# Kernel tuning notes

Hardware: AMD Instinct MI355X
Metric: run time of the kernel (lower is better)

Reference implementation:

```python
import jax, jax.numpy as jnp
import numpy as np


def _leaky(x):
    return jnp.where(x > 0, x, 0.2 * x)


def _time_warp(x, strength, k_wp, k_sh):
    # Vectorized equivalent of the per-sample python loop in _apply_time_warp.
    B, L, Fd = x.shape
    warp_steps = (L * 0.1 * strength).astype(jnp.int32)
    wp = jax.random.randint(k_wp, (B, 1), warp_steps, L - warp_steps)
    sh = jax.random.randint(k_sh, (B, 1), -warp_steps, warp_steps + 1)
    t = jnp.arange(L)[None, :]
    # shift > 0: warped[t] = x[min(t+shift, L-1)] for t >= warp_point, else x[t]
    pos = jnp.where(t >= wp, jnp.minimum(t + sh, L - 1), t)
    # shift < 0: warped[t] = x[t - shift] for warp_point+shift <= t < L+shift, else x[t]
    neg = jnp.where((t >= wp + sh) & (t < L + sh), t - sh, t)
    idx = jnp.where(sh > 0, pos, jnp.where(sh < 0, neg, t))  # (B, L)
    warped = x[jnp.arange(B)[:, None], idx]  # gather along time -> (B, L, Fd)
    return warped


def _freq_aug(x, strength, k_f):
    fx = jnp.fft.fft(x, axis=1)
    ratio = jnp.minimum(strength * 0.1, 0.5)
    keep = jax.random.uniform(k_f, x.shape) > ratio
    res = jnp.fft.ifft(fx * keep.astype(fx.dtype), axis=1).real.astype(x.dtype)
    return jnp.where(strength < 0.01, x, res)


def _forward(x, batch_size, w1, b1, w2, b2, w3, b3, wm, bm, wn, bn, ws, bs,
             p_mask, p_noise, p_shift, p_scale):
    B, L, Fd = x.shape
    s_mask = jax.nn.sigmoid(p_mask)
    s_noise = jax.nn.sigmoid(p_noise)
    s_shift = jax.nn.sigmoid(p_shift)
    s_scale = jax.nn.sigmoid(p_scale)
    s_mix = 1.0 - s_shift

    key = jax.random.key(42)
    kz, kn, kwp, ksh, kf = jax.random.split(key, 5)

    z = jax.random.normal(kz, (B, w1.shape[0]), x.dtype)
    h = _leaky(z @ w1 + b1)
    h = _leaky(h @ w2 + b2)
    h = _leaky(h @ w3 + b3)  # (B, 2*hidden)

    mask = jax.nn.sigmoid(h @ wm + bm).reshape(B, L, Fd)
    mask = 1.0 - (1.0 - mask) * s_mask * 0.3

    noise_mag = jax.nn.softplus(h @ wn + bn).reshape(B, L, Fd)
    noise = jax.random.normal(kn, x.shape, x.dtype) * noise_mag * s_noise * 0.05

    warped = _time_warp(x, s_shift, kwp, ksh)

    scale = jax.nn.softplus(h @ ws + bs)[:, None, :]  # (B,1,Fd)
    scale = 1.0 + (scale - 0.5) * 0.2 * s_scale

    freq = _freq_aug(x, s_mix, kf)

    wa = jnp.clip(1.0 - s_mix - s_shift, 0.1, 0.8)
    wb = s_mix * 0.5
    wc = s_shift * 0.5
    tot = wa + wb + wc
    wa, wb, wc = wa / tot, wb / tot, wc / tot

    aug = x * mask * scale + noise
    aug = aug * wa + freq * wb + warped * wc
    return aug


def setup_inputs() -> dict:
    key = jax.random.key(0)
    ks = jax.random.split(key, 8)
    B, L, Fd = 256, 512, 64
    H, ND = 128, 64
    x = jax.random.normal(ks[0], (B, L, Fd), jnp.float32)

    def lin(k, i, o):
        return jax.random.normal(k, (i, o), jnp.float32) * 0.02

    inp = {
        "x": x,
        "batch_size": B,
        "w1": lin(ks[1], ND, H), "b1": jnp.zeros((H,), jnp.float32),
        "w2": lin(ks[2], H, 2 * H), "b2": jnp.zeros((2 * H,), jnp.float32),
        "w3": lin(ks[3], 2 * H, 2 * H), "b3": jnp.zeros((2 * H,), jnp.float32),
        "wm": lin(ks[4], 2 * H, L * Fd), "bm": jnp.zeros((L * Fd,), jnp.float32),
        "wn": lin(ks[5], 2 * H, L * Fd), "bn": jnp.zeros((L * Fd,), jnp.float32),
        "ws": lin(ks[6], 2 * H, Fd), "bs": jnp.zeros((Fd,), jnp.float32),
        "p_mask": jnp.float32(0.5), "p_noise": jnp.float32(0.5),
        "p_shift": jnp.float32(0.5), "p_scale": jnp.float32(0.5),
    }
    return inp


def reference(x, batch_size, w1, b1, w2, b2, w3, b3, wm, bm, wn, bn, ws, bs,
              p_mask, p_noise, p_shift, p_scale):
    return _forward(x, batch_size, w1, b1, w2, b2, w3, b3, wm, bm, wn, bn,
                    ws, bs, p_mask, p_noise, p_shift, p_scale)
```

## Files before the change

kernel.cpp:

```cpp
#include <hip/hip_runtime.h>
#include <cstdint>
#include <cstddef>


typedef unsigned int u32;
typedef unsigned short u16;

#define Bd 256
#define Ld 512
#define Fd 64
#define Nd 32768

struct U2 { u32 a, b; };

__device__ __forceinline__ u32 rotl32(u32 x, int r){ return (x << r) | (x >> (32 - r)); }

__device__ __forceinline__ U2 tf2x32(u32 k0, u32 k1, u32 x0, u32 x1){
  u32 ks2 = k0 ^ k1 ^ 0x1BD11BDAu;
  x0 += k0; x1 += k1;
#define TFR4(r0,r1,r2,r3) \
  x0 += x1; x1 = rotl32(x1, r0); x1 ^= x0; \
  x0 += x1; x1 = rotl32(x1, r1); x1 ^= x0; \
  x0 += x1; x1 = rotl32(x1, r2); x1 ^= x0; \
  x0 += x1; x1 = rotl32(x1, r3); x1 ^= x0;
  TFR4(13,15,26,6)  x0 += k1;  x1 += ks2 + 1u;
  TFR4(17,29,16,24) x0 += ks2; x1 += k0 + 2u;
  TFR4(13,15,26,6)  x0 += k0;  x1 += k1 + 3u;
  TFR4(17,29,16,24) x0 += k1;  x1 += ks2 + 4u;
  TFR4(13,15,26,6)  x0 += ks2; x1 += k0 + 5u;
#undef TFR4
  U2 r; r.a = x0; r.b = x1; return r;
}

__device__ __forceinline__ u32 rb32(u32 k0, u32 k1, u32 i){
  U2 r = tf2x32(k0, k1, 0u, i);
  return r.a ^ r.b;
}

__device__ __forceinline__ U2 split_key(u32 k0, u32 k1, u32 j){
  return tf2x32(k0, k1, 0u, j);
}

__device__ __forceinline__ float sigmoidf_(float x){ return 1.0f / (1.0f + expf(-x)); }
__device__ __forceinline__ float softplusf_(float x){ return fmaxf(x, 0.0f) + log1pf(expf(-fabsf(x))); }
__device__ __forceinline__ float leakyf_(float x){ return (x > 0.0f) ? x : 0.2f * x; }

__device__ __forceinline__ float erfinvf_(float x){
  float w = -log1pf(-x * x);
  float p;
  if (w < 5.0f){
    w -= 2.5f;
    p =               2.81022636e-08f;
    p = fmaf(p, w,    3.43273939e-07f);
    p = fmaf(p, w,   -3.5233877e-06f);
    p = fmaf(p, w,   -4.39150654e-06f);
    p = fmaf(p, w,    0.00021858087f);
    p = fmaf(p, w,   -0.00125372503f);
    p = fmaf(p, w,   -0.00417768164f);
    p = fmaf(p, w,    0.246640727f);
    p = fmaf(p, w,    1.50140941f);
  } else {
    w = sqrtf(w) - 3.0f;
    p =              -0.000200214257f;
    p = fmaf(p, w,    0.000100950558f);
    p = fmaf(p, w,    0.00134934322f);
    p = fmaf(p, w,   -0.00367342844f);
    p = fmaf(p, w,    0.00573950773f);
    p = fmaf(p, w,   -0.0076224613f);
    p = fmaf(p, w,    0.00943887047f);
    p = fmaf(p, w,    1.00167406f);
    p = fmaf(p, w,    2.83297682f);
  }
  return p * x;
}

__device__ __forceinline__ float uniform_from_bits(u32 bits){
  return __uint_as_float((bits >> 9) | 0x3f800000u) - 1.0f;
}

__device__ __forceinline__ float normal_from_bits(u32 bits){
  float u01 = uniform_from_bits(bits);
  const float lo = -0.99999994f;
  float v = fmaf(u01, 2.0f, lo);
  v = fmaxf(lo, v);
  return 1.41421356f * erfinvf_(v);
}

__device__ __forceinline__ int warp_idx_(int t, int wp, int sh){
  int tps = t + sh;
  int pos = (t >= wp) ? ((tps < Ld - 1) ? tps : (Ld - 1)) : t;
  int neg = ((t >= wp + sh) && (t < Ld + sh)) ? (t - sh) : t;
  return (sh > 0) ? pos : ((sh < 0) ? neg : t);
}

__device__ __forceinline__ u32 pack_bf16_2(float a, float b){
  u32 ua = __float_as_uint(a), ub = __float_as_uint(b);
  u32 ra = (ua + 0x7FFFu + ((ua >> 16) & 1u)) >> 16;
  u32 rb = (ub + 0x7FFFu + ((ub >> 16) & 1u)) >> 16;
  return (ra & 0xFFFFu) | (rb << 16);
}
__device__ __forceinline__ u16 f2bf(float a){
  u32 ua = __float_as_uint(a);
  return (u16)((ua + 0x7FFFu + ((ua >> 16) & 1u)) >> 16);
}
__device__ __forceinline__ float bf2f(u16 v){
  return __uint_as_float(((u32)v) << 16);
}

__device__ __forceinline__ int swz_(int v){
  return ((v >> 2) & 7) ^ ((v & 3) << 1);
}
__device__ __forceinline__ int rev9_(int k){
  return (int)(__brev((u32)k) >> 23);
}

__global__ __launch_bounds__(256) void k_mlp(
    const float* __restrict__ w1, const float* __restrict__ b1,
    const float* __restrict__ w2, const float* __restrict__ b2,
    const float* __restrict__ w3, const float* __restrict__ b3,
    const float* __restrict__ wsc, const float* __restrict__ bsc,
    const float* __restrict__ p_scale, const float* __restrict__ p_shift,
    u16* __restrict__ h3b, float* __restrict__ scl,
    int* __restrict__ wp, int* __restrict__ shv)
{
  __shared__ float zs[64];
  __shared__ float h1s[128];
  __shared__ float h2s[256];
  __shared__ float hs[256];
  int b = blockIdx.x, n = threadIdx.x;

  if (n < 64){
    U2 kz = split_key(0u, 42u, 0u);
    zs[n] = normal_from_bits(rb32(kz.a, kz.b, (u32)(b * 64 + n)));
  }
  __syncthreads();

  if (n < 128){
    float acc = b1[n];
    #pragma unroll 8
    for (int k = 0; k < 64; ++k) acc = fmaf(zs[k], w1[k * 128 + n], acc);
    h1s[n] = leakyf_(acc);
  }
  __syncthreads();

  {
    float acc = b2[n];
    #pragma unroll 8
    for (int k = 0; k < 128; ++k) acc = fmaf(h1s[k], w2[k * 256 + n], acc);
    h2s[n] = leakyf_(acc);
  }
  __syncthreads();

  {
    float acc = b3[n];
    #pragma unroll 8
    for (int k = 0; k < 256; ++k) acc = fmaf(h2s[k], w3[k * 256 + n], acc);
    u16 hv = f2bf(leakyf_(acc));
    h3b[b * 256 + n] = hv;
    hs[n] = bf2f(hv);
  }
  __syncthreads();

  if (n < 64){
    float a2 = bsc[n];
    for (int k = 0; k < 256; ++k) a2 = fmaf(hs[k], wsc[k * 64 + n], a2);
    float s_scale = sigmoidf_(p_scale[0]);
    scl[b * 64 + n] = 1.0f + (softplusf_(a2) - 0.5f) * 0.2f * s_scale;
  }

  if (b < 2 && n < 128){
    int bb = b * 128 + n;
    float s_shift = sigmoidf_(p_shift[0]);
    int wsteps = (int)(51.2f * s_shift);
    U2 kwp = split_key(0u, 42u, 2u);
    U2 ksh = split_key(0u, 42u, 3u);
    {
      U2 k1 = split_key(kwp.a, kwp.b, 0u);
      U2 k2 = split_key(kwp.a, kwp.b, 1u);
      u32 hi = rb32(k1.a, k1.b, (u32)bb);
      u32 lo = rb32(k2.a, k2.b, (u32)bb);
      u32 span = (u32)(Ld - 2 * wsteps);
      u32 mult = 65536u % span; mult = (mult * mult) % span;
      u32 off = ((hi % span) * mult + (lo % span)) % span;
      wp[bb] = wsteps + (int)off;
    }
    {
      U2 k1 = split_key(ksh.a, ksh.b, 0u);
      U2 k2 = split_key(ksh.a, ksh.b, 1u);
      u32 hi = rb32(k1.a, k1.b, (u32)bb);
      u32 lo = rb32(k2.a, k2.b, (u32)bb);
      u32 span = (u32)(2 * wsteps + 1);
      u32 mult = 65536u % span; mult = (mult * mult) % span;
      u32 off = ((hi % span) * mult + (lo % span)) % span;
      shv[bb] = -wsteps + (int)off;
    }
  }
}

typedef short short8 __attribute__((ext_vector_type(8)));
typedef float f32x4 __attribute__((ext_vector_type(4)));
union Frag { uint4 u; short8 s; };

__global__ __launch_bounds__(256, 2) void k_gemm(
    const u16* __restrict__ h3b,
    const float* __restrict__ wm, const float* __restrict__ bm,
    const float* __restrict__ wn, const float* __restrict__ bn,
    u32* __restrict__ mn)
{
  __shared__ __align__(16) u32 As [128 * 32];
  __shared__ __align__(16) u32 Bs0[128 * 32];
  __shared__ __align__(16) u32 Bs1[128 * 32];

  const int tid  = threadIdx.x;
  const int lane = tid & 63;
  const int w    = tid >> 6;
  const int q    = lane >> 4;
  const int lo   = lane & 15;
  const int nt0  = blockIdx.x << 7;
  const int b0   = blockIdx.y << 7;
  const int wr   = (w >> 1) << 6;
  const int wc   = (w & 1) << 6;

  const int p  = lane >> 3;
  const int c8 = lane & 7;
  const int nb = (w << 5) + (p << 2);

  f32x4 accm[4][4], accn[4][4];
  #pragma unroll
  for (int i = 0; i < 4; ++i)
    #pragma unroll
    for (int j = 0; j < 4; ++j){ accm[i][j] = (f32x4)0.0f; accn[i][j] = (f32x4)0.0f; }

  for (int kc = 0; kc < 256; kc += 64){
    if (kc) __syncthreads();
    #pragma unroll
    for (int j = 0; j < 4; ++j){
      int idx  = j * 256 + tid;
      int row  = idx >> 3;
      int slot = idx & 7;
      int g    = slot ^ swz_(row);
      uint4 v  = *(const uint4*)(h3b + (size_t)(b0 + row) * 256 + kc + g * 8);
      *(uint4*)&As[row * 32 + slot * 4] = v;
    }
    #pragma unroll
    for (int cp = 0; cp < 4; ++cp){
      int c = cp * 8 + c8;
      size_t gb = (size_t)(kc + 2 * c) * Nd + nt0 + nb;
      float4 m0 = *(const float4*)(wm + gb);
      float4 m1 = *(const float4*)(wm + gb + Nd);
      float4 v0 = *(const float4*)(wn + gb);
      float4 v1 = *(const float4*)(wn + gb + Nd);
      int g = c >> 2, cl = c & 3;
      #pragma unroll
      for (int s = 0; s < 4; ++s){
        int n = nb + s;
        int addr = n * 32 + (g ^ swz_(n)) * 4 + cl;
        float a0 = (s == 0) ? m0.x : (s == 1) ? m0.y : (s == 2) ? m0.z : m0.w;
        float a1 = (s == 0) ? m1.x : (s == 1) ? m1.y : (s == 2) ? m1.z : m1.w;
        float b0f = (s == 0) ? v0.x : (s == 1) ? v0.y : (s == 2) ? v0.z : v0.w;
        float b1f = (s == 0) ? v1.x : (s == 1) ? v1.y : (s == 2) ? v1.z : v1.w;
        Bs0[addr] = pack_bf16_2(a0, a1);
        Bs1[addr] = pack_bf16_2(b0f, b1f);
      }
    }
    __syncthreads();

    #pragma unroll
    for (int u = 0; u < 2; ++u){
      int G = u * 4 + q;
      Frag af[4], bfm[4], bfn[4];
      #pragma unroll
      for (int mt = 0; mt < 4; ++mt){
        int row = wr + mt * 16 + lo;
        af[mt].u = *(const uint4*)&As[row * 32 + (G ^ swz_(row)) * 4];
      }
      #pragma unroll
      for (int nt = 0; nt < 4; ++nt){
        int n = wc + nt * 16 + lo;
        int ad = n * 32 + (G ^ swz_(n)) * 4;
        bfm[nt].u = *(const uint4*)&Bs0[ad];
        bfn[nt].u = *(const uint4*)&Bs1[ad];
      }
      #pragma unroll
      for (int mt = 0; mt < 4; ++mt){
        #pragma unroll
        for (int nt = 0; nt < 4; ++nt){
          accm[mt][nt] = __builtin_amdgcn_mfma_f32_16x16x32_bf16(af[mt].s, bfm[nt].s, accm[mt][nt], 0, 0, 0);
          accn[mt][nt] = __builtin_amdgcn_mfma_f32_16x16x32_bf16(af[mt].s, bfn[nt].s, accn[mt][nt], 0, 0, 0);
        }
      }
    }
  }

  #pragma unroll
  for (int nt = 0; nt < 4; ++nt){
    int n = nt0 + wc + nt * 16 + lo;
    float bmv = bm[n];
    float bnv = bn[n];
    #pragma unroll
    for (int mt = 0; mt < 4; ++mt){
      #pragma unroll
      for (int r = 0; r < 4; ++r){
        int b = b0 + wr + mt * 16 + q * 4 + r;
        size_t o = (size_t)b * Nd + n;
        mn[o] = pack_bf16_2(accm[mt][nt][r] + bmv, accn[mt][nt][r] + bnv);
      }
    }
  }
}

__global__ __launch_bounds__(256) void k_noise(u32* __restrict__ mn,
                                               const float* __restrict__ p_noise){
  int gid = blockIdx.x * 256 + threadIdx.x;
  u32 base = (u32)gid * 8u;
  float s_noise = sigmoidf_(p_noise[0]);
  float sc = s_noise * 0.05f;
  U2 knk = split_key(0u, 42u, 1u);

  uint4 v0 = *(const uint4*)(mn + base);
  uint4 v1 = *(const uint4*)(mn + base + 4);
  u32 wds[8] = {v0.x, v0.y, v0.z, v0.w, v1.x, v1.y, v1.z, v1.w};
  #pragma unroll
  for (int h = 0; h < 8; ++h){
    u16 logit = (u16)(wds[h] >> 16);
    float nm = softplusf_(bf2f(logit));
    float nz = normal_from_bits(rb32(knk.a, knk.b, base + (u32)h));
    wds[h] = (wds[h] & 0xFFFFu) | ((u32)f2bf(nz * nm * sc) << 16);
  }
  *(uint4*)(mn + base)     = make_uint4(wds[0], wds[1], wds[2], wds[3]);
  *(uint4*)(mn + base + 4) = make_uint4(wds[4], wds[5], wds[6], wds[7]);
}

#define PITCH 529

__device__ __forceinline__ int lphys(int t){ return t + (t >> 5); }

__global__ __launch_bounds__(256, 4) void k_faug(
    const float* __restrict__ x,
    u32* mn,
    const float* __restrict__ scl,
    const int* __restrict__ wp, const int* __restrict__ shv,
    const float* __restrict__ p_mask, const float* __restrict__ p_noise,
    const float* __restrict__ p_shift)
{
  __shared__ float SR[8 * PITCH];
  __shared__ float SI[8 * PITCH];
  __shared__ float2 tw[256];

  const int tid = threadIdx.x;
  const int b   = blockIdx.x >> 2;
  const int f0  = (blockIdx.x & 3) << 4;

  float s_mask  = sigmoidf_(p_mask[0]);
  float s_shift = sigmoidf_(p_shift[0]);
  float s_mix   = 1.0f - s_shift;
  float ratio   = fminf(s_mix * 0.1f, 0.5f);
  float wa = 1.0f - s_mix - s_shift;
  wa = fminf(fmaxf(wa, 0.1f), 0.8f);
  float wb = s_mix * 0.5f;
  float wc = s_shift * 0.5f;
  float tot = wa + wb + wc;
  wa /= tot; wb /= tot; wc /= tot;
  bool pass = (s_mix < 0.01f);
  (void)p_noise;

  U2 kf  = split_key(0u, 42u, 4u);
  const int wpb = wp[b];
  const int shb = shv[b];

  {
    float ang = -6.283185307179586f * ((float)tid / 512.0f);
    tw[tid] = make_float2(cosf(ang), sinf(ang));
  }

  const float* xb = x + (size_t)b * Nd;
  #pragma unroll
  for (int s = 0; s < 8; ++s){
    int qq = (s << 8) + tid;
    int t  = qq >> 2;
    int f4 = qq & 3;
    float4 v = *(const float4*)(xb + t * 64 + f0 + (f4 << 2));
    int j = f4 << 1;
    int pt = lphys(t);
    SR[j * PITCH + pt]       = v.x;  SI[j * PITCH + pt]       = v.y;
    SR[(j + 1) * PITCH + pt] = v.z;  SI[(j + 1) * PITCH + pt] = v.w;
  }
  __syncthreads();

  for (int s = 9; s >= 1; --s){
    int half = 1 << (s - 1);
    #pragma unroll
    for (int it = 0; it < 8; ++it){
      int j  = it;
      int bi = tid;
      int pos = bi & (half - 1);
      int g = bi >> (s - 1);
      int i1 = (g << s) + pos;
      int i2 = i1 + half;
      int a1 = j * PITCH + lphys(i1);
      int a2 = j * PITCH + lphys(i2);
      float ur = SR[a1], ui = SI[a1];
      float vr = SR[a2], vi = SI[a2];
      SR[a1] = ur + vr; SI[a1] = ui + vi;
      float dr = ur - vr, di = ui - vi;
      float2 w = tw[pos << (9 - s)];
      SR[a2] = dr * w.x - di * w.y;
      SI[a2] = dr * w.y + di * w.x;
    }
    __syncthreads();
  }

  #pragma unroll
  for (int it = 0; it < 8; ++it){
    int j = it;
    int k = tid;
    int nItr = (k == 0) ? 2 : 1;
    for (int e = 0; e < nItr; ++e){
      int kk = (e == 0) ? k : 256;
      int nk = (512 - kk) & 511;
      int pk = rev9_(kk), pn = rev9_(nk);
      int ak = j * PITCH + lphys(pk);
      int an = j * PITCH + lphys(pn);
      float zkr = SR[ak], zki = SI[ak];
      float znr = SR[an], zni = SI[an];
      float X0r = 0.5f * (zkr + znr), X0i = 0.5f * (zki - zni);
      float X1r = 0.5f * (zki + zni), X1i = 0.5f * (znr - zkr);
      int fA = f0 + (j << 1);
      u32 ck = (u32)((b * Ld + kk) * Fd + fA);
      u32 cn = (u32)((b * Ld + nk) * Fd + fA);
      float k0a = (uniform_from_bits(rb32(kf.a, kf.b, ck))      > ratio) ? 1.0f : 0.0f;
      float k0b = (uniform_from_bits(rb32(kf.a, kf.b, cn))      > ratio) ? 1.0f : 0.0f;
      float k1a = (uniform_from_bits(rb32(kf.a, kf.b, ck + 1u)) > ratio) ? 1.0f : 0.0f;
      float k1b = (uniform_from_bits(rb32(kf.a, kf.b, cn + 1u)) > ratio) ? 1.0f : 0.0f;
      float m0 = 0.5f * (k0a + k0b);
      float m1 = 0.5f * (k1a + k1b);
      SR[ak] = m0 * X0r - m1 * X1i;
      SI[ak] = m0 * X0i + m1 * X1r;
      SR[an] = m0 * X0r + m1 * X1i;
      SI[an] = m1 * X1r - m0 * X0i;
    }
  }
  __syncthreads();

  for (int s = 1; s <= 9; ++s){
    int half = 1 << (s - 1);
    #pragma unroll
    for (int it = 0; it < 8; ++it){
      int j  = it;
      int bi = tid;
      int pos = bi & (half - 1);
      int g = bi >> (s - 1);
      int i1 = (g << s) + pos;
      int i2 = i1 + half;
      int a1 = j * PITCH + lphys(i1);
      int a2 = j * PITCH + lphys(i2);
      float2 w = tw[pos << (9 - s)];
      float vr = SR[a2], vi = SI[a2];
      float tx_ = vr * w.x + vi * w.y;
      float ty_ = vi * w.x - vr * w.y;
      float ur = SR[a1], ui = SI[a1];
      SR[a1] = ur + tx_; SI[a1] = ui + ty_;
      SR[a2] = ur - tx_; SI[a2] = ui - ty_;
    }
    __syncthreads();
  }

  const float inv512 = 1.0f / 512.0f;
  u32* mnb = mn + (size_t)b * Nd;
  #pragma unroll
  for (int s = 0; s < 8; ++s){
    int qq = (s << 8) + tid;
    int t  = qq >> 2;
    int f4 = qq & 3;
    int f  = f0 + (f4 << 2);
    int j  = f4 << 1;
    int pt = lphys(t);
    int nidx = t * 64 + f;
    float4 xv = *(const float4*)(xb + nidx);
    int wi = warp_idx_(t, wpb, shb);
    float4 wv = *(const float4*)(xb + wi * 64 + f);
    float4 sc = *(const float4*)(scl + b * 64 + f);
    uint4 w4 = *(const uint4*)(mnb + nidx);
    float fr[4];
    fr[0] = SR[j * PITCH + pt] * inv512;
    fr[1] = SI[j * PITCH + pt] * inv512;
    fr[2] = SR[(j + 1) * PITCH + pt] * inv512;
    fr[3] = SI[(j + 1) * PITCH + pt] * inv512;
    const float xvv[4] = {xv.x, xv.y, xv.z, xv.w};
    const float wvv[4] = {wv.x, wv.y, wv.z, wv.w};
    const float scv[4] = {sc.x, sc.y, sc.z, sc.w};
    const u32 wdv[4] = {w4.x, w4.y, w4.z, w4.w};
    float o[4];
    #pragma unroll
    for (int c = 0; c < 4; ++c){
      float maskv = sigmoidf_(bf2f((u16)(wdv[c] & 0xFFFFu)));
      maskv = 1.0f - (1.0f - maskv) * s_mask * 0.3f;
      float noise = bf2f((u16)(wdv[c] >> 16));
      float fq = pass ? xvv[c] : fr[c];
      float aug = fmaf(xvv[c] * maskv, scv[c], noise);
      o[c] = aug * wa + fq * wb + wvv[c] * wc;
    }
    *(float4*)(mnb + nidx) = make_float4(o[0], o[1], o[2], o[3]);
  }
}

extern "C" void kernel_launch(void* const* d_in, const int* in_sizes, int n_in,
                              void* d_out, int out_size, void* d_ws, size_t ws_size,
                              hipStream_t stream)
{
  (void)in_sizes; (void)n_in; (void)out_size; (void)ws_size;
  const float* x   = (const float*)d_in[0];
  const float* w1  = (const float*)d_in[2];
  const float* b1  = (const float*)d_in[3];
  const float* w2  = (const float*)d_in[4];
  const float* b2  = (const float*)d_in[5];
  const float* w3  = (const float*)d_in[6];
  const float* b3  = (const float*)d_in[7];
  const float* wm  = (const float*)d_in[8];
  const float* bm  = (const float*)d_in[9];
  const float* wn  = (const float*)d_in[10];
  const float* bn  = (const float*)d_in[11];
  const float* wsc = (const float*)d_in[12];
  const float* bsc = (const float*)d_in[13];
  const float* pm  = (const float*)d_in[14];
  const float* pn  = (const float*)d_in[15];
  const float* psh = (const float*)d_in[16];
  const float* psc = (const float*)d_in[17];
  char* ws = (char*)d_ws;

  int*   wp   = (int*)(ws + 0);
  int*   shv  = (int*)(ws + 1024);
  u16*   h3b  = (u16*)(ws + 4096);
  float* scl  = (float*)(ws + 4096 + 131072);
  u32*   mn   = (u32*)d_out;

  k_mlp  <<<dim3(256),     dim3(256), 0, stream>>>(w1, b1, w2, b2, w3, b3,
                                                   wsc, bsc, psc, psh,
                                                   h3b, scl, wp, shv);
  k_gemm <<<dim3(256, 2),  dim3(256), 0, stream>>>(h3b, wm, bm, wn, bn, mn);
  k_noise<<<dim3(4096),    dim3(256), 0, stream>>>(mn, pn);
  k_faug <<<dim3(1024),    dim3(256), 0, stream>>>(x, mn, scl, wp, shv,
                                                   pm, pn, psh);
}
```

Baseline: 315.3 us.

## Precompute frequency keep-mask in MLP kernel and halve FFT block width

Moves the Threefry-based frequency keep-mask generation out of the FFT kernel into extra blocks of the MLP kernel, which write a packed byte per bin pair to workspace. The FFT kernel then reads these bytes instead of computing four hashes per element. Each FFT block now handles 8 feature columns instead of 16, halving shared memory so more blocks fit per CU (launch bounds raised to 6), and the grid doubles. This trades extra global traffic for the mask array and a larger MLP launch against less ALU work and better occupancy in the FFT kernel.

Measured after the change: 334.2 us. 6.0% more time.

```diff
diff --git a/kernel.cpp b/kernel.cpp
--- a/kernel.cpp
+++ b/kernel.cpp
@@ -5,6 +5,7 @@
 
 typedef unsigned int u32;
 typedef unsigned short u16;
+typedef unsigned char u8;
 
 #define Bd 256
 #define Ld 512
@@ -121,13 +122,40 @@
     const float* __restrict__ wsc, const float* __restrict__ bsc,
     const float* __restrict__ p_scale, const float* __restrict__ p_shift,
     u16* __restrict__ h3b, float* __restrict__ scl,
-    int* __restrict__ wp, int* __restrict__ shv)
+    int* __restrict__ wp, int* __restrict__ shv,
+    u8* __restrict__ fm)
 {
   __shared__ float zs[64];
   __shared__ float h1s[128];
   __shared__ float h2s[256];
   __shared__ float hs[256];
-  int b = blockIdx.x, n = threadIdx.x;
+  const int bid = blockIdx.x;
+  const int n = threadIdx.x;
+
+  {
+    int fb = bid >> 5;
+    int jf = bid & 31;
+    int fA = jf << 1;
+    float s_shift = sigmoidf_(p_shift[0]);
+    float s_mix = 1.0f - s_shift;
+    float ratio = fminf(s_mix * 0.1f, 0.5f);
+    U2 kf = split_key(0u, 42u, 4u);
+    int nItr = (n == 0) ? 2 : 1;
+    for (int e = 0; e < nItr; ++e){
+      int kk = (e == 0) ? n : 256;
+      int nk = (512 - kk) & 511;
+      u32 ck = (u32)((fb * Ld + kk) * Fd + fA);
+      u32 cn = (u32)((fb * Ld + nk) * Fd + fA);
+      int k0a = (uniform_from_bits(rb32(kf.a, kf.b, ck))      > ratio) ? 1 : 0;
+      int k0b = (uniform_from_bits(rb32(kf.a, kf.b, cn))      > ratio) ? 1 : 0;
+      int k1a = (uniform_from_bits(rb32(kf.a, kf.b, ck + 1u)) > ratio) ? 1 : 0;
+      int k1b = (uniform_from_bits(rb32(kf.a, kf.b, cn + 1u)) > ratio) ? 1 : 0;
+      fm[(size_t)bid * 257 + kk] = (u8)((k0a + k0b) | ((k1a + k1b) << 2));
+    }
+  }
+
+  if (bid >= 256) return;
+  const int b = bid;
 
   if (n < 64){
     U2 kz = split_key(0u, 42u, 0u);
@@ -335,26 +363,25 @@
 
 __device__ __forceinline__ int lphys(int t){ return t + (t >> 5); }
 
-__global__ __launch_bounds__(256, 4) void k_faug(
+__global__ __launch_bounds__(256, 6) void k_faug(
     const float* __restrict__ x,
     u32* mn,
     const float* __restrict__ scl,
     const int* __restrict__ wp, const int* __restrict__ shv,
-    const float* __restrict__ p_mask, const float* __restrict__ p_noise,
-    const float* __restrict__ p_shift)
+    const u8* __restrict__ fm,
+    const float* __restrict__ p_mask, const float* __restrict__ p_shift)
 {
-  __shared__ float SR[8 * PITCH];
-  __shared__ float SI[8 * PITCH];
+  __shared__ float SR[4 * PITCH];
+  __shared__ float SI[4 * PITCH];
   __shared__ float2 tw[256];
 
   const int tid = threadIdx.x;
-  const int b   = blockIdx.x >> 2;
-  const int f0  = (blockIdx.x & 3) << 4;
+  const int b   = blockIdx.x >> 3;
+  const int f0  = (blockIdx.x & 7) << 3;
 
   float s_mask  = sigmoidf_(p_mask[0]);
   float s_shift = sigmoidf_(p_shift[0]);
   float s_mix   = 1.0f - s_shift;
-  float ratio   = fminf(s_mix * 0.1f, 0.5f);
   float wa = 1.0f - s_mix - s_shift;
   wa = fminf(fmaxf(wa, 0.1f), 0.8f);
   float wb = s_mix * 0.5f;
@@ -362,9 +389,7 @@
   float tot = wa + wb + wc;
   wa /= tot; wb /= tot; wc /= tot;
   bool pass = (s_mix < 0.01f);
-  (void)p_noise;
-
-  U2 kf  = split_key(0u, 42u, 4u);
+
   const int wpb = wp[b];
   const int shb = shv[b];
 
@@ -375,10 +400,10 @@
 
   const float* xb = x + (size_t)b * Nd;
   #pragma unroll
-  for (int s = 0; s < 8; ++s){
+  for (int s = 0; s < 4; ++s){
     int qq = (s << 8) + tid;
-    int t  = qq >> 2;
-    int f4 = qq & 3;
+    int t  = qq >> 1;
+    int f4 = qq & 1;
     float4 v = *(const float4*)(xb + t * 64 + f0 + (f4 << 2));
     int j = f4 << 1;
     int pt = lphys(t);
@@ -390,7 +415,7 @@
   for (int s = 9; s >= 1; --s){
     int half = 1 << (s - 1);
     #pragma unroll
-    for (int it = 0; it < 8; ++it){
+    for (int it = 0; it < 4; ++it){
       int j  = it;
       int bi = tid;
       int pos = bi & (half - 1);
@@ -410,34 +435,31 @@
     __syncthreads();
   }
 
-  #pragma unroll
-  for (int it = 0; it < 8; ++it){
-    int j = it;
-    int k = tid;
-    int nItr = (k == 0) ? 2 : 1;
-    for (int e = 0; e < nItr; ++e){
-      int kk = (e == 0) ? k : 256;
-      int nk = (512 - kk) & 511;
-      int pk = rev9_(kk), pn = rev9_(nk);
-      int ak = j * PITCH + lphys(pk);
-      int an = j * PITCH + lphys(pn);
-      float zkr = SR[ak], zki = SI[ak];
-      float znr = SR[an], zni = SI[an];
-      float X0r = 0.5f * (zkr + znr), X0i = 0.5f * (zki - zni);
-      float X1r = 0.5f * (zki + zni), X1i = 0.5f * (znr - zkr);
-      int fA = f0 + (j << 1);
-      u32 ck = (u32)((b * Ld + kk) * Fd + fA);
-      u32 cn = (u32)((b * Ld + nk) * Fd + fA);
-      float k0a = (uniform_from_bits(rb32(kf.a, kf.b, ck))      > ratio) ? 1.0f : 0.0f;
-      float k0b = (uniform_from_bits(rb32(kf.a, kf.b, cn))      > ratio) ? 1.0f : 0.0f;
-      float k1a = (uniform_from_bits(rb32(kf.a, kf.b, ck + 1u)) > ratio) ? 1.0f : 0.0f;
-      float k1b = (uniform_from_bits(rb32(kf.a, kf.b, cn + 1u)) > ratio) ? 1.0f : 0.0f;
-      float m0 = 0.5f * (k0a + k0b);
-      float m1 = 0.5f * (k1a + k1b);
-      SR[ak] = m0 * X0r - m1 * X1i;
-      SI[ak] = m0 * X0i + m1 * X1r;
-      SR[an] = m0 * X0r + m1 * X1i;
-      SI[an] = m1 * X1r - m0 * X0i;
+  {
+    const u8* fmb = fm + ((size_t)((b << 5) + (f0 >> 1))) * 257;
+    #pragma unroll
+    for (int it = 0; it < 4; ++it){
+      int j = it;
+      int k = tid;
+      int nItr = (k == 0) ? 2 : 1;
+      for (int e = 0; e < nItr; ++e){
+        int kk = (e == 0) ? k : 256;
+        int nk = (512 - kk) & 511;
+        int pk = rev9_(kk), pn = rev9_(nk);
+        int ak = j * PITCH + lphys(pk);
+        int an = j * PITCH + lphys(pn);
+        float zkr = SR[ak], zki = SI[ak];
+        float znr = SR[an], zni = SI[an];
+        float X0r = 0.5f * (zkr + znr), X0i = 0.5f * (zki - zni);
+        float X1r = 0.5f * (zki + zni), X1i = 0.5f * (znr - zkr);
+        u8 mq = fmb[j * 257 + kk];
+        float m0 = 0.5f * (float)(mq & 3);
+        float m1 = 0.5f * (float)(mq >> 2);
+        SR[ak] = m0 * X0r - m1 * X1i;
+        SI[ak] = m0 * X0i + m1 * X1r;
+        SR[an] = m0 * X0r + m1 * X1i;
+        SI[an] = m1 * X1r - m0 * X0i;
+      }
     }
   }
   __syncthreads();
@@ -445,7 +467,7 @@
   for (int s = 1; s <= 9; ++s){
     int half = 1 << (s - 1);
     #pragma unroll
-    for (int it = 0; it < 8; ++it){
+    for (int it = 0; it < 4; ++it){
       int j  = it;
       int bi = tid;
       int pos = bi & (half - 1);
@@ -468,10 +490,10 @@
   const float inv512 = 1.0f / 512.0f;
   u32* mnb = mn + (size_t)b * Nd;
   #pragma unroll
-  for (int s = 0; s < 8; ++s){
+  for (int s = 0; s < 4; ++s){
     int qq = (s << 8) + tid;
-    int t  = qq >> 2;
-    int f4 = qq & 3;
+    int t  = qq >> 1;
+    int f4 = qq & 1;
     int f  = f0 + (f4 << 2);
     int j  = f4 << 1;
     int pt = lphys(t);
@@ -532,13 +554,14 @@
   int*   shv  = (int*)(ws + 1024);
   u16*   h3b  = (u16*)(ws + 4096);
   float* scl  = (float*)(ws + 4096 + 131072);
+  u8*    fm   = (u8*) (ws + 4096 + 131072 + 65536);
   u32*   mn   = (u32*)d_out;
 
-  k_mlp  <<<dim3(256),     dim3(256), 0, stream>>>(w1, b1, w2, b2, w3, b3,
+  k_mlp  <<<dim3(8192),    dim3(256), 0, stream>>>(w1, b1, w2, b2, w3, b3,
                                                    wsc, bsc, psc, psh,
-                                                   h3b, scl, wp, shv);
+                                                   h3b, scl, wp, shv, fm);
   k_gemm <<<dim3(256, 2),  dim3(256), 0, stream>>>(h3b, wm, bm, wn, bn, mn);
   k_noise<<<dim3(4096),    dim3(256), 0, stream>>>(mn, pn);
-  k_faug <<<dim3(1024),    dim3(256), 0, stream>>>(x, mn, scl, wp, shv,
-                                                   pm, pn, psh);
-}
+  k_faug <<<dim3(2048),    dim3(256), 0, stream>>>(x, mn, scl, wp, shv, fm,
+                                                   pm, psh);
+}
```
